# Kernel optimization log

Measured on AMD Instinct MI355X. Metric: run time of the kernel, lower is better.

The kernel has to match this reference:

```python
import jax, jax.numpy as jnp
import numpy as np

# Model constants (match init_kwargs + mamba_ssm defaults)
CIN, COUT, K, STRIDE = 64, 128, 4, 4
D = 128            # d_model = features_out
DI = 256           # d_inner = 2*D (expand=2)
NSTATE = 16        # d_state
DCONV = 4          # depthwise conv width
DT_RANK = 8        # ceil(D/16)
NB = 3             # blocks per direction
NTOT = 2 * NB      # forward + backward stacks


def setup_inputs() -> dict:
    key = jax.random.key(0)
    ks = jax.random.split(key, 10)
    s = 0.02
    x = jax.random.normal(ks[0], (2, CIN, 8192), jnp.float32)
    convd_w = jax.random.normal(ks[1], (COUT, CIN, K), jnp.float32) * s
    convd_b = jnp.zeros((COUT,), jnp.float32)
    ln_w = jnp.ones((NTOT, D), jnp.float32)
    ln_b = jnp.zeros((NTOT, D), jnp.float32)
    in_proj_w = jax.random.normal(ks[2], (NTOT, 2 * DI, D), jnp.float32) * s
    conv_w = jax.random.normal(ks[3], (NTOT, DI, DCONV), jnp.float32) * s
    conv_b = jnp.zeros((NTOT, DI), jnp.float32)
    xproj_w = jax.random.normal(ks[4], (NTOT, DT_RANK + 2 * NSTATE, DI), jnp.float32) * s
    dtproj_w = jax.random.normal(ks[5], (NTOT, DI, DT_RANK), jnp.float32) * s
    dtproj_b = jax.random.normal(ks[6], (NTOT, DI), jnp.float32) * s
    # S4D-real init: A = -[1..N]
    A_log = jnp.log(jnp.broadcast_to(jnp.arange(1, NSTATE + 1, dtype=jnp.float32), (NTOT, DI, NSTATE)))
    Dparam = jnp.ones((NTOT, DI), jnp.float32)
    outproj_w = jax.random.normal(ks[7], (NTOT, D, DI), jnp.float32) * s
    return dict(x=x, convd_w=convd_w, convd_b=convd_b, ln_w=ln_w, ln_b=ln_b,
                in_proj_w=in_proj_w, conv_w=conv_w, conv_b=conv_b, xproj_w=xproj_w,
                dtproj_w=dtproj_w, dtproj_b=dtproj_b, A_log=A_log, Dparam=Dparam,
                outproj_w=outproj_w)


def _silu(x):
    return x * jax.nn.sigmoid(x)


def _layernorm(x, w, b, eps=1e-5):
    m = x.mean(-1, keepdims=True)
    xc = x - m
    v = (xc * xc).mean(-1, keepdims=True)
    return xc * jax.lax.rsqrt(v + eps) * w + b


def _mamba_mixer(x, in_proj_w, conv_w, conv_b, xproj_w, dtproj_w, dtproj_b, A_log, Dp, outproj_w):
    # x: (B, L, D)
    B, L, _ = x.shape
    xz = jnp.einsum('bld,ed->ble', x, in_proj_w)          # (B, L, 2*DI)
    xm, z = jnp.split(xz, 2, axis=-1)
    # causal depthwise conv (pad left DCONV-1, truncate to L)
    xp = jnp.pad(xm, ((0, 0), (DCONV - 1, 0), (0, 0)))
    xc = conv_b
    acc = jnp.zeros_like(xm)
    for k in range(DCONV):
        acc = acc + xp[:, k:k + L, :] * conv_w[:, k]
    xc = _silu(acc + conv_b)                               # (B, L, DI)
    dbc = jnp.einsum('ble,ne->bln', xc, xproj_w)           # (B, L, DT_RANK + 2N)
    dt, Bc, Cc = jnp.split(dbc, [DT_RANK, DT_RANK + NSTATE], axis=-1)
    dt = jax.nn.softplus(jnp.einsum('blr,dr->bld', dt, dtproj_w) + dtproj_b)  # (B, L, DI)
    A = -jnp.exp(A_log)                                    # (DI, N)
    dA = jnp.exp(dt[..., None] * A)                        # (B, L, DI, N)
    dBx = dt[..., None] * Bc[:, :, None, :] * xc[..., None]

    def step(h, inp):
        dA_t, dBx_t, C_t = inp
        h = dA_t * h + dBx_t                               # (B, DI, N)
        y = jnp.einsum('bdn,bn->bd', h, C_t)
        return h, y

    h0 = jnp.zeros((B, DI, NSTATE), x.dtype)
    _, ys = jax.lax.scan(step, h0, (jnp.swapaxes(dA, 0, 1), jnp.swapaxes(dBx, 0, 1), jnp.swapaxes(Cc, 0, 1)))
    y = jnp.swapaxes(ys, 0, 1)                             # (B, L, DI)
    y = (y + Dp * xc) * _silu(z)
    return jnp.einsum('ble,de->bld', y, outproj_w)         # (B, L, D)


def _mamba_stack(x, off, ln_w, ln_b, in_proj_w, conv_w, conv_b, xproj_w, dtproj_w, dtproj_b, A_log, Dparam, outproj_w):
    # mamba_ssm Block semantics: residual = x (+ prev residual); x = mixer(norm(residual))
    res = None
    cur = x
    for i in range(NB):
        j = off + i
        res = cur if res is None else cur + res
        hn = _layernorm(res, ln_w[j], ln_b[j])
        cur = _mamba_mixer(hn, in_proj_w[j], conv_w[j], conv_b[j], xproj_w[j],
                           dtproj_w[j], dtproj_b[j], A_log[j], Dparam[j], outproj_w[j])
    return cur, res


def reference(x, convd_w, convd_b, ln_w, ln_b, in_proj_w, conv_w, conv_b, xproj_w,
              dtproj_w, dtproj_b, A_log, Dparam, outproj_w):
    # downsampling conv + SiLU
    y = jax.lax.conv_general_dilated(x, convd_w, (STRIDE,), 'VALID',
                                     dimension_numbers=('NCH', 'OIH', 'NCH'))
    y = _silu(y + convd_b[None, :, None])                  # (B, COUT, L')
    h = jnp.swapaxes(y, 1, 2)                              # (B, L', D)
    xf, rf = _mamba_stack(h, 0, ln_w, ln_b, in_proj_w, conv_w, conv_b, xproj_w,
                          dtproj_w, dtproj_b, A_log, Dparam, outproj_w)
    xb, rb = _mamba_stack(h[:, ::-1, :], NB, ln_w, ln_b, in_proj_w, conv_w, conv_b, xproj_w,
                          dtproj_w, dtproj_b, A_log, Dparam, outproj_w)
    out = (xf + rf) + (xb + rb)[:, ::-1, :]
    return jnp.swapaxes(out, 1, 2), rf, rb
```

## Files before the change

kernel.cpp:

```cpp
#include <hip/hip_runtime.h>
#include <hip/hip_bf16.h>
#include <math.h>

#define B    2
#define CIN  64
#define LIN  8192
#define L    2048
#define D    128
#define DI   256
#define NS   16
#define RK   8
#define NSTREAM 4
#define CH   32
#define NCH  (L/CH)
#define TOK  (NSTREAM*L)
#define SZ_D ((size_t)TOK*D)
#define SZ_DI ((size_t)TOK*DI)
#define SXM 280
#define SHN 152

typedef short  bfrag __attribute__((ext_vector_type(8)));
typedef float  facc  __attribute__((ext_vector_type(4)));
#define MFMA __builtin_amdgcn_mfma_f32_16x16x32_bf16

__device__ __forceinline__ float sigmoidf_(float x){ return 1.f/(1.f+__expf(-x)); }
__device__ __forceinline__ float siluf_(float x){ return x*sigmoidf_(x); }
__device__ __forceinline__ ushort f2bf(float f){
    unsigned u = __float_as_uint(f);
    u += 0x7fffu + ((u>>16)&1u);
    return (ushort)(u>>16);
}
__device__ __forceinline__ float bf2f(ushort u){ return __uint_as_float(((unsigned)u)<<16); }
__device__ __forceinline__ float softplusf_(float t){
    return (t > 20.f) ? t : __logf(1.f + __expf(t));
}

__global__ void k_cvtall(const float* __restrict__ cw, const float* __restrict__ ipw,
                         const float* __restrict__ opw, const float* __restrict__ xpw,
                         ushort* __restrict__ dst){
    int i = blockIdx.x*256 + threadIdx.x;
    ushort v;
    if (i < 32768)       v = f2bf(cw[i]);
    else if (i < 425984) v = f2bf(ipw[i-32768]);
    else if (i < 622592) v = f2bf(opw[i-425984]);
    else {
        int t = i - 622592;
        int k = t & 255, nr = (t>>8) & 63, j = t>>14;
        v = (nr < 40) ? f2bf(xpw[((size_t)j*40 + nr)*256 + k]) : (ushort)0;
    }
    dst[i] = v;
}

__global__ void k_down(const float* __restrict__ x, const ushort* __restrict__ wd,
                       const float* __restrict__ bias, float* __restrict__ h){
    __shared__ ushort sxd[64*SXM];
    int tid = threadIdx.x;
    int m0 = blockIdx.x*64;
    int b = m0 >> 11;
    int l0 = m0 & 2047;
    for (int idx = tid; idx < 64*64; idx += 256){
        int t = idx & 63, cc = idx >> 6;
        float4 v = *(const float4*)(x + ((size_t)(b*CIN + cc))*LIN + 4*(l0+t));
        ushort4 o; o.x=f2bf(v.x); o.y=f2bf(v.y); o.z=f2bf(v.z); o.w=f2bf(v.w);
        *(ushort4*)&sxd[t*SXM + cc*4] = o;
    }
    __syncthreads();
    int w = tid>>6, lane = tid&63, rw = w>>1, cw = w&1;
    int q = lane>>4, r = lane&15;
    int n0 = blockIdx.y*64 + cw*32;
    const ushort* b0p = wd + (size_t)(n0 + r)*256 + q*8;
    const ushort* b1p = b0p + (size_t)16*256;
    facc acc[2][2] = {};
    #pragma unroll
    for (int kb=0; kb<8; ++kb){
        bfrag a0 = *(bfrag*)&sxd[(rw*32 + r)*SXM + kb*32 + q*8];
        bfrag a1 = *(bfrag*)&sxd[(rw*32 + 16 + r)*SXM + kb*32 + q*8];
        bfrag b0 = *(const bfrag*)(b0p + kb*32);
        bfrag b1 = *(const bfrag*)(b1p + kb*32);
        acc[0][0] = MFMA(a0,b0,acc[0][0],0,0,0);
        acc[0][1] = MFMA(a0,b1,acc[0][1],0,0,0);
        acc[1][0] = MFMA(a1,b0,acc[1][0],0,0,0);
        acc[1][1] = MFMA(a1,b1,acc[1][1],0,0,0);
    }
    #pragma unroll
    for (int im=0; im<2; ++im)
    #pragma unroll
    for (int in=0; in<2; ++in){
        int col = n0 + in*16 + r;
        float bv = bias[col];
        #pragma unroll
        for (int r2=0; r2<4; ++r2){
            int row = m0 + rw*32 + im*16 + q*4 + r2;
            int bb = row >> 11, l = row & 2047;
            float v = siluf_(acc[im][in][r2] + bv);
            h[((size_t)(bb*L + l))*D + col] = v;
            h[((size_t)((2+bb)*L + (L-1-l)))*D + col] = v;
        }
    }
}

__global__ void __launch_bounds__(256,1)
k_head(const float* __restrict__ curIn, const float* __restrict__ resIn,
       float* __restrict__ resOut,
       const float* __restrict__ lnw, const float* __restrict__ lnb,
       const ushort* __restrict__ wbi, const ushort* __restrict__ wbx,
       const float* __restrict__ cw, const float* __restrict__ cb,
       const float* __restrict__ Wdt, const float* __restrict__ bdt,
       const float* __restrict__ A_log,
       float* __restrict__ z, float* __restrict__ xc,
       float* __restrict__ dtr, float* __restrict__ Bc, float* __restrict__ Cc,
       float* __restrict__ Aprod, float* __restrict__ Bend, int blk, int first){
    __shared__ ushort smHn[35*SHN];
    __shared__ ushort smXm[35*SXM];
    __shared__ ushort smXc[32*SXM];
    __shared__ float  smDbc[32*68];
    const int tid = threadIdx.x;
    const int bi = blockIdx.x;
    const int s = bi >> 6, c = bi & 63;
    const int j = (s>>1)*3 + blk;
    const int base_tok = s*L + c*CH;

    {
        int t = tid >> 3, g8 = tid & 7;
        size_t off = (size_t)(base_tok + t)*D + g8*16;
        float4 v[4];
        const float4* cp = (const float4*)(curIn + off);
        #pragma unroll
        for (int i=0;i<4;++i) v[i] = cp[i];
        if (!first){
            const float4* rp = (const float4*)(resIn + off);
            #pragma unroll
            for (int i=0;i<4;++i){ float4 rv=rp[i]; v[i].x+=rv.x; v[i].y+=rv.y; v[i].z+=rv.z; v[i].w+=rv.w; }
        }
        {
            float4* ro = (float4*)(resOut + off);
            #pragma unroll
            for (int i=0;i<4;++i) ro[i] = v[i];
        }
        float s1=0.f, s2=0.f;
        #pragma unroll
        for (int i=0;i<4;++i){
            s1 += v[i].x+v[i].y+v[i].z+v[i].w;
            s2 += v[i].x*v[i].x+v[i].y*v[i].y+v[i].z*v[i].z+v[i].w*v[i].w;
        }
        s1 += __shfl_xor(s1,1); s2 += __shfl_xor(s2,1);
        s1 += __shfl_xor(s1,2); s2 += __shfl_xor(s2,2);
        s1 += __shfl_xor(s1,4); s2 += __shfl_xor(s2,4);
        float mean = s1*(1.f/128.f);
        float var  = s2*(1.f/128.f) - mean*mean;
        float rstd = rsqrtf(var + 1e-5f);
        const float4* lwp = (const float4*)(lnw + j*D + g8*16);
        const float4* lbp = (const float4*)(lnb + j*D + g8*16);
        #pragma unroll
        for (int i=0;i<4;++i){
            float4 lw = lwp[i], lb = lbp[i];
            ushort4 o;
            o.x = f2bf((v[i].x-mean)*rstd*lw.x + lb.x);
            o.y = f2bf((v[i].y-mean)*rstd*lw.y + lb.y);
            o.z = f2bf((v[i].z-mean)*rstd*lw.z + lb.z);
            o.w = f2bf((v[i].w-mean)*rstd*lw.w + lb.w);
            *(ushort4*)&smHn[t*SHN + g8*16 + i*4] = o;
        }
    }
    if (c > 0 && tid < 24){
        int t = tid >> 3, g8 = tid & 7;
        size_t off = (size_t)(base_tok - 3 + t)*D + g8*16;
        float4 v[4];
        const float4* cp = (const float4*)(curIn + off);
        #pragma unroll
        for (int i=0;i<4;++i) v[i] = cp[i];
        if (!first){
            const float4* rp = (const float4*)(resIn + off);
            #pragma unroll
            for (int i=0;i<4;++i){ float4 rv=rp[i]; v[i].x+=rv.x; v[i].y+=rv.y; v[i].z+=rv.z; v[i].w+=rv.w; }
        }
        float s1=0.f, s2=0.f;
        #pragma unroll
        for (int i=0;i<4;++i){
            s1 += v[i].x+v[i].y+v[i].z+v[i].w;
            s2 += v[i].x*v[i].x+v[i].y*v[i].y+v[i].z*v[i].z+v[i].w*v[i].w;
        }
        s1 += __shfl_xor(s1,1); s2 += __shfl_xor(s2,1);
        s1 += __shfl_xor(s1,2); s2 += __shfl_xor(s2,2);
        s1 += __shfl_xor(s1,4); s2 += __shfl_xor(s2,4);
        float mean = s1*(1.f/128.f);
        float var  = s2*(1.f/128.f) - mean*mean;
        float rstd = rsqrtf(var + 1e-5f);
        const float4* lwp = (const float4*)(lnw + j*D + g8*16);
        const float4* lbp = (const float4*)(lnb + j*D + g8*16);
        #pragma unroll
        for (int i=0;i<4;++i){
            float4 lw = lwp[i], lb = lbp[i];
            ushort4 o;
            o.x = f2bf((v[i].x-mean)*rstd*lw.x + lb.x);
            o.y = f2bf((v[i].y-mean)*rstd*lw.y + lb.y);
            o.z = f2bf((v[i].z-mean)*rstd*lw.z + lb.z);
            o.w = f2bf((v[i].w-mean)*rstd*lw.w + lb.w);
            *(ushort4*)&smHn[(32+t)*SHN + g8*16 + i*4] = o;
        }
    }
    __syncthreads();

    {
        int w = tid>>6, lane = tid&63, q = lane>>4, r = lane&15;
        bfrag a[3][4];
        #pragma unroll
        for (int rt=0; rt<3; ++rt)
        #pragma unroll
        for (int kb=0; kb<4; ++kb)
            a[rt][kb] = *(bfrag*)&smHn[(rt*16 + r)*SHN + kb*32 + q*8];
        #pragma unroll
        for (int ct=0; ct<8; ++ct){
            int n0 = w*128 + ct*16;
            const ushort* bp = wbi + ((size_t)j*512 + n0 + r)*128 + q*8;
            facc a0 = {}, a1 = {}, a2 = {};
            #pragma unroll
            for (int kb=0; kb<4; ++kb){
                bfrag bv = *(const bfrag*)(bp + kb*32);
                a0 = MFMA(a[0][kb], bv, a0, 0,0,0);
                a1 = MFMA(a[1][kb], bv, a1, 0,0,0);
                a2 = MFMA(a[2][kb], bv, a2, 0,0,0);
            }
            int colL = n0 + r;
            if (colL < DI){
                #pragma unroll
                for (int r2=0;r2<4;++r2){
                    int rr = q*4 + r2;
                    smXm[rr*SXM + colL]      = f2bf(a0[r2]);
                    smXm[(16+rr)*SXM + colL] = f2bf(a1[r2]);
                    if (rr < 3) smXm[(32+rr)*SXM + colL] = f2bf(a2[r2]);
                }
            } else {
                int cz = colL - DI;
                #pragma unroll
                for (int r2=0;r2<4;++r2){
                    int rr = q*4 + r2;
                    z[(size_t)(base_tok + rr)*DI + cz]      = a0[r2];
                    z[(size_t)(base_tok + 16 + rr)*DI + cz] = a1[r2];
                }
            }
        }
    }
    __syncthreads();

    {
        const float* w4 = cw + ((size_t)j*DI + tid)*4;
        float cw0=w4[0], cw1=w4[1], cw2=w4[2], cw3=w4[3];
        float cbb = cb[j*DI + tid];
        float xm1=0.f, xm2=0.f, xm3=0.f;
        if (c > 0){
            xm3 = bf2f(smXm[32*SXM + tid]);
            xm2 = bf2f(smXm[33*SXM + tid]);
            xm1 = bf2f(smXm[34*SXM + tid]);
        }
        #pragma unroll 4
        for (int i=0;i<CH;++i){
            float x0 = bf2f(smXm[i*SXM + tid]);
            float v = siluf_(cbb + cw3*x0 + cw2*xm1 + cw1*xm2 + cw0*xm3);
            smXc[i*SXM + tid] = f2bf(v);
            xc[(size_t)(base_tok+i)*DI + tid] = v;
            xm3 = xm2; xm2 = xm1; xm1 = x0;
        }
    }
    __syncthreads();

    {
        int w = tid>>6, lane = tid&63, q = lane>>4, r = lane&15;
        facc a0 = {}, a1 = {};
        const ushort* bp = wbx + ((size_t)j*64 + w*16 + r)*256 + q*8;
        #pragma unroll
        for (int kb=0; kb<8; ++kb){
            bfrag av0 = *(bfrag*)&smXc[r*SXM + kb*32 + q*8];
            bfrag av1 = *(bfrag*)&smXc[(16+r)*SXM + kb*32 + q*8];
            bfrag bv  = *(const bfrag*)(bp + kb*32);
            a0 = MFMA(av0, bv, a0, 0,0,0);
            a1 = MFMA(av1, bv, a1, 0,0,0);
        }
        int col = w*16 + r;
        #pragma unroll
        for (int r2=0;r2<4;++r2){
            int rr = q*4 + r2;
            smDbc[rr*68 + col]      = a0[r2];
            smDbc[(16+rr)*68 + col] = a1[r2];
            int row0 = base_tok + rr, row1 = base_tok + 16 + rr;
            if      (col < 8){  dtr[(size_t)row0*RK + col] = a0[r2];      dtr[(size_t)row1*RK + col] = a1[r2]; }
            else if (col < 24){ Bc [(size_t)row0*NS + (col-8)] = a0[r2];  Bc [(size_t)row1*NS + (col-8)] = a1[r2]; }
            else if (col < 40){ Cc [(size_t)row0*NS + (col-24)] = a0[r2]; Cc [(size_t)row1*NS + (col-24)] = a1[r2]; }
        }
    }
    __syncthreads();

    {
        float A[NS], wv[RK];
        const float* ar = A_log + ((size_t)j*DI + tid)*NS;
        #pragma unroll
        for (int n=0;n<NS;++n) A[n] = -__expf(ar[n]);
        const float* wr = Wdt + ((size_t)j*DI + tid)*RK;
        #pragma unroll
        for (int r=0;r<RK;++r) wv[r] = wr[r];
        float bb2 = bdt[j*DI + tid];
        float ap[NS], hs[NS];
        #pragma unroll
        for (int n=0;n<NS;++n){ ap[n]=1.f; hs[n]=0.f; }
        #pragma unroll 4
        for (int l=0;l<CH;++l){
            float t = bb2;
            #pragma unroll
            for (int r=0;r<RK;++r) t += smDbc[l*68+r]*wv[r];
            float dtv = softplusf_(t);
            float xv  = bf2f(smXc[l*SXM + tid]);
            float dbx = dtv*xv;
            #pragma unroll
            for (int n=0;n<NS;++n){
                float dA = __expf(dtv*A[n]);
                ap[n] *= dA;
                hs[n] = dA*hs[n] + dbx*smDbc[l*68+8+n];
            }
        }
        size_t pb = (size_t)bi*4096 + tid;
        #pragma unroll
        for (int n=0;n<NS;++n){
            Aprod[pb + (size_t)n*256] = ap[n];
            Bend [pb + (size_t)n*256] = hs[n];
        }
    }
}

__global__ void k_scanmid(const float* __restrict__ Aprod, float* __restrict__ Bend){
    int tid = blockIdx.x*128 + threadIdx.x;
    int s = tid >> 12;
    int nd = tid & 4095;
    size_t base = (size_t)s*NCH*4096 + nd;
    float h = 0.f;
    for (int c0=0; c0<NCH; c0+=16){
        float a[16], b[16];
        #pragma unroll
        for (int i=0;i<16;++i){
            a[i] = Aprod[base + (size_t)(c0+i)*4096];
            b[i] = Bend [base + (size_t)(c0+i)*4096];
        }
        #pragma unroll
        for (int i=0;i<16;++i){
            Bend[base + (size_t)(c0+i)*4096] = h;
            h = a[i]*h + b[i];
        }
    }
}

__global__ void k_tail(const float* __restrict__ dtr, const float* __restrict__ xcv,
                       const float* __restrict__ Bc, const float* __restrict__ Cc,
                       const float* __restrict__ A_log,
                       const float* __restrict__ Wdt, const float* __restrict__ bdt,
                       const float* __restrict__ h0, const float* __restrict__ z,
                       const float* __restrict__ Dp, const ushort* __restrict__ wbo,
                       float* __restrict__ cur, int blk){
    int c = blockIdx.x, s = blockIdx.y; int j = (s>>1)*3 + blk;
    int d = threadIdx.x;
    __shared__ float sB[CH*NS], sC[CH*NS], sdtr[CH*RK];
    __shared__ ushort sg[CH*SXM];
    int base_tok = s*L + c*CH;
    sB[d] = Bc[(size_t)base_tok*NS + d];
    sB[256+d] = Bc[(size_t)base_tok*NS + 256 + d];
    sC[d] = Cc[(size_t)base_tok*NS + d];
    sC[256+d] = Cc[(size_t)base_tok*NS + 256 + d];
    sdtr[d] = dtr[(size_t)base_tok*RK + d];
    float A[NS], wv[RK];
    const float* ar = A_log + ((size_t)j*DI + d)*NS;
    #pragma unroll
    for (int n=0;n<NS;++n) A[n] = -__expf(ar[n]);
    const float* wr = Wdt + ((size_t)j*DI + d)*RK;
    #pragma unroll
    for (int r=0;r<RK;++r) wv[r] = wr[r];
    float bb = bdt[j*DI + d];
    float Dpd = Dp[j*DI + d];
    float hs[NS];
    size_t pb = (size_t)(s*NCH + c)*4096 + d;
    #pragma unroll
    for (int n=0;n<NS;++n) hs[n] = h0[pb + (size_t)n*256];
    __syncthreads();
    #pragma unroll 4
    for (int l=0;l<CH;++l){
        float t = bb;
        #pragma unroll
        for (int r=0;r<RK;++r) t += sdtr[l*RK+r]*wv[r];
        float dtv = softplusf_(t);
        float xv  = xcv[(size_t)(base_tok+l)*DI + d];
        float dbx = dtv*xv;
        float p = 0.f;
        #pragma unroll
        for (int n=0;n<NS;++n){
            float dA = __expf(dtv*A[n]);
            hs[n] = dA*hs[n] + dbx*sB[l*NS+n];
            p += hs[n]*sC[l*NS+n];
        }
        float zv = z[(size_t)(base_tok+l)*DI + d];
        sg[l*SXM + d] = f2bf((p + Dpd*xv)*siluf_(zv));
    }
    __syncthreads();
    int w = d>>6, lane = d&63, q = lane>>4, r = lane&15;
    facc acc[2][2] = {};
    const ushort* b0p = wbo + ((size_t)j*128 + w*32 + r)*256 + q*8;
    const ushort* b1p = b0p + 16*256;
    #pragma unroll
    for (int kb=0; kb<8; ++kb){
        bfrag av0 = *(bfrag*)&sg[r*SXM + kb*32 + q*8];
        bfrag av1 = *(bfrag*)&sg[(16+r)*SXM + kb*32 + q*8];
        bfrag bv0 = *(const bfrag*)(b0p + kb*32);
        bfrag bv1 = *(const bfrag*)(b1p + kb*32);
        acc[0][0] = MFMA(av0,bv0,acc[0][0],0,0,0);
        acc[0][1] = MFMA(av0,bv1,acc[0][1],0,0,0);
        acc[1][0] = MFMA(av1,bv0,acc[1][0],0,0,0);
        acc[1][1] = MFMA(av1,bv1,acc[1][1],0,0,0);
    }
    #pragma unroll
    for (int rt=0; rt<2; ++rt)
    #pragma unroll
    for (int ct=0; ct<2; ++ct){
        int col = w*32 + ct*16 + r;
        #pragma unroll
        for (int r2=0;r2<4;++r2){
            int row = base_tok + rt*16 + q*4 + r2;
            cur[(size_t)row*D + col] = acc[rt][ct][r2];
        }
    }
}

__global__ void k_final(const float* __restrict__ cur, const float* __restrict__ res,
                        float* __restrict__ out){
    int l = blockIdx.x, b = blockIdx.y, d = threadIdx.x;
    int tf = (b*L + l)*D + d;
    int tbk = ((2+b)*L + (L-1-l))*D + d;
    float f  = cur[tf] + res[tf];
    float bw = cur[tbk] + res[tbk];
    out[((size_t)(b*D + d))*L + l] = f + bw;
    out[(size_t)2*D*L + (size_t)(b*L + l)*D + d] = res[tf];
    out[(size_t)2*D*L + (size_t)((2+b)*L + l)*D + d] = res[((2+b)*L + l)*D + d];
}

extern "C" void kernel_launch(void* const* d_in, const int* in_sizes, int n_in,
                              void* d_out, int out_size, void* d_ws, size_t ws_size,
                              hipStream_t stream){
    const float* x         = (const float*)d_in[0];
    const float* convd_w   = (const float*)d_in[1];
    const float* convd_b   = (const float*)d_in[2];
    const float* ln_w      = (const float*)d_in[3];
    const float* ln_b      = (const float*)d_in[4];
    const float* in_proj_w = (const float*)d_in[5];
    const float* conv_w    = (const float*)d_in[6];
    const float* conv_b    = (const float*)d_in[7];
    const float* xproj_w   = (const float*)d_in[8];
    const float* dtproj_w  = (const float*)d_in[9];
    const float* dtproj_b  = (const float*)d_in[10];
    const float* A_log     = (const float*)d_in[11];
    const float* Dparam    = (const float*)d_in[12];
    const float* outproj_w = (const float*)d_in[13];

    float* ws = (float*)d_ws;
    float* h     = ws; ws += SZ_D;
    float* res0  = ws; ws += SZ_D;
    float* res1  = ws; ws += SZ_D;
    float* cur   = ws; ws += SZ_D;
    float* z     = ws; ws += SZ_DI;
    float* xc    = ws; ws += SZ_DI;
    float* Aprod = ws; ws += SZ_D;
    float* Bend  = ws; ws += SZ_D;
    float* dtr   = ws; ws += (size_t)TOK*RK;
    float* Bc    = ws; ws += (size_t)TOK*NS;
    float* Cc    = ws; ws += (size_t)TOK*NS;
    ushort* wall = (ushort*)ws;
    ushort* wbd  = wall;
    ushort* wbi  = wall + 32768;
    ushort* wbo  = wall + 425984;
    ushort* wbx  = wall + 622592;

    k_cvtall<<<2816, 256, 0, stream>>>(convd_w, in_proj_w, outproj_w, xproj_w, wall);
    k_down<<<dim3(64, 2), 256, 0, stream>>>(x, wbd, convd_b, h);

    float* resin[3]  = { nullptr, res0, res1 };
    float* resout[3] = { res0,    res1, res0 };
    for (int blk = 0; blk < 3; ++blk){
        const float* ci = (blk==0) ? h : cur;
        const float* ri = (blk==0) ? h : resin[blk];
        k_head<<<NSTREAM*NCH, 256, 0, stream>>>(ci, ri, resout[blk], ln_w, ln_b, wbi, wbx,
                                                conv_w, conv_b, dtproj_w, dtproj_b, A_log,
                                                z, xc, dtr, Bc, Cc, Aprod, Bend, blk, blk==0);
        k_scanmid<<<128, 128, 0, stream>>>(Aprod, Bend);
        k_tail<<<dim3(NCH, NSTREAM), 256, 0, stream>>>(dtr, xc, Bc, Cc, A_log,
                                                       dtproj_w, dtproj_b, Bend, z,
                                                       Dparam, wbo, cur, blk);
    }

    k_final<<<dim3(L, B), 128, 0, stream>>>(cur, res0, (float*)d_out);
}
```

Before: 254.4 us.

## Fuse downsample conv into first head, store z/xc as bf16, tile final transpose

Removes the separate k_down kernel and instead computes the strided downsampling conv plus SiLU inside k_head on the first block. Each chunk recomputes its own tokens plus a 3-token halo in shared memory, for both directions, so the h buffer is never written or read. The z and conv-output intermediates are stored as bf16 rather than fp32, halving their traffic, and k_tail preloads them into registers. k_final is rewritten with a shared-memory transpose for coalesced output writes and a vectorized residual copy. The trade-offs are redundant halo computation, bf16 rounding of z/xc that could shift accuracy, and higher register pressure in k_tail.

```diff
diff --git a/kernel.cpp b/kernel.cpp
--- a/kernel.cpp
+++ b/kernel.cpp
@@ -51,86 +51,90 @@
     dst[i] = v;
 }
 
-__global__ void k_down(const float* __restrict__ x, const ushort* __restrict__ wd,
-                       const float* __restrict__ bias, float* __restrict__ h){
-    __shared__ ushort sxd[64*SXM];
-    int tid = threadIdx.x;
-    int m0 = blockIdx.x*64;
-    int b = m0 >> 11;
-    int l0 = m0 & 2047;
-    for (int idx = tid; idx < 64*64; idx += 256){
-        int t = idx & 63, cc = idx >> 6;
-        float4 v = *(const float4*)(x + ((size_t)(b*CIN + cc))*LIN + 4*(l0+t));
-        ushort4 o; o.x=f2bf(v.x); o.y=f2bf(v.y); o.z=f2bf(v.z); o.w=f2bf(v.w);
-        *(ushort4*)&sxd[t*SXM + cc*4] = o;
-    }
-    __syncthreads();
-    int w = tid>>6, lane = tid&63, rw = w>>1, cw = w&1;
-    int q = lane>>4, r = lane&15;
-    int n0 = blockIdx.y*64 + cw*32;
-    const ushort* b0p = wd + (size_t)(n0 + r)*256 + q*8;
-    const ushort* b1p = b0p + (size_t)16*256;
-    facc acc[2][2] = {};
-    #pragma unroll
-    for (int kb=0; kb<8; ++kb){
-        bfrag a0 = *(bfrag*)&sxd[(rw*32 + r)*SXM + kb*32 + q*8];
-        bfrag a1 = *(bfrag*)&sxd[(rw*32 + 16 + r)*SXM + kb*32 + q*8];
-        bfrag b0 = *(const bfrag*)(b0p + kb*32);
-        bfrag b1 = *(const bfrag*)(b1p + kb*32);
-        acc[0][0] = MFMA(a0,b0,acc[0][0],0,0,0);
-        acc[0][1] = MFMA(a0,b1,acc[0][1],0,0,0);
-        acc[1][0] = MFMA(a1,b0,acc[1][0],0,0,0);
-        acc[1][1] = MFMA(a1,b1,acc[1][1],0,0,0);
-    }
-    #pragma unroll
-    for (int im=0; im<2; ++im)
-    #pragma unroll
-    for (int in=0; in<2; ++in){
-        int col = n0 + in*16 + r;
-        float bv = bias[col];
-        #pragma unroll
-        for (int r2=0; r2<4; ++r2){
-            int row = m0 + rw*32 + im*16 + q*4 + r2;
-            int bb = row >> 11, l = row & 2047;
-            float v = siluf_(acc[im][in][r2] + bv);
-            h[((size_t)(bb*L + l))*D + col] = v;
-            h[((size_t)((2+bb)*L + (L-1-l)))*D + col] = v;
-        }
-    }
-}
-
 __global__ void __launch_bounds__(256,1)
-k_head(const float* __restrict__ curIn, const float* __restrict__ resIn,
+k_head(const float* __restrict__ x,
+       const float* __restrict__ curIn, const float* __restrict__ resIn,
        float* __restrict__ resOut,
        const float* __restrict__ lnw, const float* __restrict__ lnb,
-       const ushort* __restrict__ wbi, const ushort* __restrict__ wbx,
+       const ushort* __restrict__ wbd, const ushort* __restrict__ wbi,
+       const ushort* __restrict__ wbx,
+       const float* __restrict__ dbias,
        const float* __restrict__ cw, const float* __restrict__ cb,
        const float* __restrict__ Wdt, const float* __restrict__ bdt,
        const float* __restrict__ A_log,
-       float* __restrict__ z, float* __restrict__ xc,
+       ushort* __restrict__ zb, ushort* __restrict__ xcb,
        float* __restrict__ dtr, float* __restrict__ Bc, float* __restrict__ Cc,
        float* __restrict__ Aprod, float* __restrict__ Bend, int blk, int first){
     __shared__ ushort smHn[35*SHN];
     __shared__ ushort smXm[35*SXM];
     __shared__ ushort smXc[32*SXM];
     __shared__ float  smDbc[32*68];
+    __shared__ float  smF[35*132];
     const int tid = threadIdx.x;
     const int bi = blockIdx.x;
     const int s = bi >> 6, c = bi & 63;
     const int j = (s>>1)*3 + blk;
     const int base_tok = s*L + c*CH;
 
+    if (first){
+        int bB = s & 1, dir = s >> 1;
+        for (int idx = tid; idx < 2240; idx += 256){
+            int rr = idx >> 6, cc = idx & 63;
+            int tl; bool valid = true;
+            if (rr < 32) tl = c*CH + rr;
+            else { tl = c*CH - 3 + (rr - 32); valid = (c > 0); }
+            if (valid){
+                int lo = dir ? (L-1-tl) : tl;
+                float4 v = *(const float4*)(x + ((size_t)(bB*CIN + cc))*LIN + 4*lo);
+                ushort4 o; o.x=f2bf(v.x); o.y=f2bf(v.y); o.z=f2bf(v.z); o.w=f2bf(v.w);
+                *(ushort4*)&smXm[rr*SXM + cc*4] = o;
+            }
+        }
+        __syncthreads();
+        int w = tid>>6, lane = tid&63, q = lane>>4, r = lane&15;
+        #pragma unroll
+        for (int ct=0; ct<2; ++ct){
+            int n0 = w*32 + ct*16;
+            const ushort* bp = wbd + (size_t)(n0 + r)*256 + q*8;
+            facc A0 = {}, A1 = {}, A2 = {};
+            #pragma unroll
+            for (int kb=0; kb<8; ++kb){
+                bfrag bv = *(const bfrag*)(bp + kb*32);
+                bfrag a0 = *(bfrag*)&smXm[r*SXM + kb*32 + q*8];
+                bfrag a1 = *(bfrag*)&smXm[(16+r)*SXM + kb*32 + q*8];
+                bfrag a2 = *(bfrag*)&smXm[(32+r)*SXM + kb*32 + q*8];
+                A0 = MFMA(a0,bv,A0,0,0,0);
+                A1 = MFMA(a1,bv,A1,0,0,0);
+                A2 = MFMA(a2,bv,A2,0,0,0);
+            }
+            float bvv = dbias[n0 + r];
+            #pragma unroll
+            for (int r2=0; r2<4; ++r2){
+                int rr2 = q*4 + r2;
+                smF[rr2*132 + n0 + r]      = siluf_(A0[r2] + bvv);
+                smF[(16+rr2)*132 + n0 + r] = siluf_(A1[r2] + bvv);
+                if (rr2 < 3) smF[(32+rr2)*132 + n0 + r] = siluf_(A2[r2] + bvv);
+            }
+        }
+        __syncthreads();
+    }
+
     {
         int t = tid >> 3, g8 = tid & 7;
         size_t off = (size_t)(base_tok + t)*D + g8*16;
         float4 v[4];
-        const float4* cp = (const float4*)(curIn + off);
-        #pragma unroll
-        for (int i=0;i<4;++i) v[i] = cp[i];
-        if (!first){
+        if (first){
+            #pragma unroll
+            for (int i=0;i<4;++i) v[i] = *(float4*)&smF[t*132 + g8*16 + i*4];
+        } else {
+            const float4* cp = (const float4*)(curIn + off);
             const float4* rp = (const float4*)(resIn + off);
             #pragma unroll
-            for (int i=0;i<4;++i){ float4 rv=rp[i]; v[i].x+=rv.x; v[i].y+=rv.y; v[i].z+=rv.z; v[i].w+=rv.w; }
+            for (int i=0;i<4;++i){
+                v[i] = cp[i];
+                float4 rv = rp[i];
+                v[i].x+=rv.x; v[i].y+=rv.y; v[i].z+=rv.z; v[i].w+=rv.w;
+            }
         }
         {
             float4* ro = (float4*)(resOut + off);
@@ -166,13 +170,18 @@
         int t = tid >> 3, g8 = tid & 7;
         size_t off = (size_t)(base_tok - 3 + t)*D + g8*16;
         float4 v[4];
-        const float4* cp = (const float4*)(curIn + off);
-        #pragma unroll
-        for (int i=0;i<4;++i) v[i] = cp[i];
-        if (!first){
+        if (first){
+            #pragma unroll
+            for (int i=0;i<4;++i) v[i] = *(float4*)&smF[(32+t)*132 + g8*16 + i*4];
+        } else {
+            const float4* cp = (const float4*)(curIn + off);
             const float4* rp = (const float4*)(resIn + off);
             #pragma unroll
-            for (int i=0;i<4;++i){ float4 rv=rp[i]; v[i].x+=rv.x; v[i].y+=rv.y; v[i].z+=rv.z; v[i].w+=rv.w; }
+            for (int i=0;i<4;++i){
+                v[i] = cp[i];
+                float4 rv = rp[i];
+                v[i].x+=rv.x; v[i].y+=rv.y; v[i].z+=rv.z; v[i].w+=rv.w;
+            }
         }
         float s1=0.f, s2=0.f;
         #pragma unroll
@@ -235,8 +244,8 @@
                 #pragma unroll
                 for (int r2=0;r2<4;++r2){
                     int rr = q*4 + r2;
-                    z[(size_t)(base_tok + rr)*DI + cz]      = a0[r2];
-                    z[(size_t)(base_tok + 16 + rr)*DI + cz] = a1[r2];
+                    zb[(size_t)(base_tok + rr)*DI + cz]      = f2bf(a0[r2]);
+                    zb[(size_t)(base_tok + 16 + rr)*DI + cz] = f2bf(a1[r2]);
                 }
             }
         }
@@ -257,8 +266,9 @@
         for (int i=0;i<CH;++i){
             float x0 = bf2f(smXm[i*SXM + tid]);
             float v = siluf_(cbb + cw3*x0 + cw2*xm1 + cw1*xm2 + cw0*xm3);
-            smXc[i*SXM + tid] = f2bf(v);
-            xc[(size_t)(base_tok+i)*DI + tid] = v;
+            ushort us = f2bf(v);
+            smXc[i*SXM + tid] = us;
+            xcb[(size_t)(base_tok+i)*DI + tid] = us;
             xm3 = xm2; xm2 = xm1; xm1 = x0;
         }
     }
@@ -347,11 +357,11 @@
     }
 }
 
-__global__ void k_tail(const float* __restrict__ dtr, const float* __restrict__ xcv,
+__global__ void k_tail(const float* __restrict__ dtr, const ushort* __restrict__ xcb,
                        const float* __restrict__ Bc, const float* __restrict__ Cc,
                        const float* __restrict__ A_log,
                        const float* __restrict__ Wdt, const float* __restrict__ bdt,
-                       const float* __restrict__ h0, const float* __restrict__ z,
+                       const float* __restrict__ h0, const ushort* __restrict__ zb,
                        const float* __restrict__ Dp, const ushort* __restrict__ wbo,
                        float* __restrict__ cur, int blk){
     int c = blockIdx.x, s = blockIdx.y; int j = (s>>1)*3 + blk;
@@ -359,11 +369,17 @@
     __shared__ float sB[CH*NS], sC[CH*NS], sdtr[CH*RK];
     __shared__ ushort sg[CH*SXM];
     int base_tok = s*L + c*CH;
-    sB[d] = Bc[(size_t)base_tok*NS + d];
+    ushort xvv[CH], zvv[CH];
+    #pragma unroll
+    for (int l=0;l<CH;++l){
+        xvv[l] = xcb[(size_t)(base_tok+l)*DI + d];
+        zvv[l] = zb [(size_t)(base_tok+l)*DI + d];
+    }
+    sB[d]     = Bc[(size_t)base_tok*NS + d];
     sB[256+d] = Bc[(size_t)base_tok*NS + 256 + d];
-    sC[d] = Cc[(size_t)base_tok*NS + d];
+    sC[d]     = Cc[(size_t)base_tok*NS + d];
     sC[256+d] = Cc[(size_t)base_tok*NS + 256 + d];
-    sdtr[d] = dtr[(size_t)base_tok*RK + d];
+    sdtr[d]   = dtr[(size_t)base_tok*RK + d];
     float A[NS], wv[RK];
     const float* ar = A_log + ((size_t)j*DI + d)*NS;
     #pragma unroll
@@ -384,7 +400,7 @@
         #pragma unroll
         for (int r=0;r<RK;++r) t += sdtr[l*RK+r]*wv[r];
         float dtv = softplusf_(t);
-        float xv  = xcv[(size_t)(base_tok+l)*DI + d];
+        float xv  = bf2f(xvv[l]);
         float dbx = dtv*xv;
         float p = 0.f;
         #pragma unroll
@@ -393,7 +409,7 @@
             hs[n] = dA*hs[n] + dbx*sB[l*NS+n];
             p += hs[n]*sC[l*NS+n];
         }
-        float zv = z[(size_t)(base_tok+l)*DI + d];
+        float zv = bf2f(zvv[l]);
         sg[l*SXM + d] = f2bf((p + Dpd*xv)*siluf_(zv));
     }
     __syncthreads();
@@ -427,14 +443,41 @@
 
 __global__ void k_final(const float* __restrict__ cur, const float* __restrict__ res,
                         float* __restrict__ out){
-    int l = blockIdx.x, b = blockIdx.y, d = threadIdx.x;
-    int tf = (b*L + l)*D + d;
-    int tbk = ((2+b)*L + (L-1-l))*D + d;
-    float f  = cur[tf] + res[tf];
-    float bw = cur[tbk] + res[tbk];
-    out[((size_t)(b*D + d))*L + l] = f + bw;
-    out[(size_t)2*D*L + (size_t)(b*L + l)*D + d] = res[tf];
-    out[(size_t)2*D*L + (size_t)((2+b)*L + l)*D + d] = res[((2+b)*L + l)*D + d];
+    __shared__ float tile[128*33];
+    int tid = threadIdx.x;
+    int c = blockIdx.x, b = blockIdx.y;
+    int t = tid>>3, g8 = tid&7;
+    int lf = c*32 + t, lb = L-1-lf;
+    size_t fo = ((size_t)(b*L + lf))*D + g8*16;
+    size_t bo = ((size_t)((2+b)*L + lb))*D + g8*16;
+    #pragma unroll
+    for (int i=0;i<4;++i){
+        float4 cf  = *(const float4*)(cur + fo + i*4);
+        float4 rf  = *(const float4*)(res + fo + i*4);
+        float4 cb2 = *(const float4*)(cur + bo + i*4);
+        float4 rb2 = *(const float4*)(res + bo + i*4);
+        int db = g8*16 + i*4;
+        tile[(db+0)*33 + t] = cf.x+rf.x+cb2.x+rb2.x;
+        tile[(db+1)*33 + t] = cf.y+rf.y+cb2.y+rb2.y;
+        tile[(db+2)*33 + t] = cf.z+rf.z+cb2.z+rb2.z;
+        tile[(db+3)*33 + t] = cf.w+rf.w+cb2.w+rb2.w;
+    }
+    __syncthreads();
+    int d = tid>>1, hf = tid&1;
+    size_t obase = ((size_t)(b*D + d))*L + c*32 + hf*16;
+    #pragma unroll
+    for (int i=0;i<4;++i){
+        float4 o4;
+        o4.x = tile[d*33 + hf*16 + i*4 + 0];
+        o4.y = tile[d*33 + hf*16 + i*4 + 1];
+        o4.z = tile[d*33 + hf*16 + i*4 + 2];
+        o4.w = tile[d*33 + hf*16 + i*4 + 3];
+        *(float4*)(out + obase + i*4) = o4;
+    }
+    const float4* src = (const float4*)res;
+    float4* dst = (float4*)(out + (size_t)2*D*L);
+    for (int idx = (blockIdx.y*NCH + blockIdx.x)*256 + tid; idx < 262144; idx += 2*NCH*256)
+        dst[idx] = src[idx];
 }
 
 extern "C" void kernel_launch(void* const* d_in, const int* in_sizes, int n_in,
@@ -456,17 +499,16 @@
     const float* outproj_w = (const float*)d_in[13];
 
     float* ws = (float*)d_ws;
-    float* h     = ws; ws += SZ_D;
     float* res0  = ws; ws += SZ_D;
     float* res1  = ws; ws += SZ_D;
     float* cur   = ws; ws += SZ_D;
-    float* z     = ws; ws += SZ_DI;
-    float* xc    = ws; ws += SZ_DI;
     float* Aprod = ws; ws += SZ_D;
     float* Bend  = ws; ws += SZ_D;
     float* dtr   = ws; ws += (size_t)TOK*RK;
     float* Bc    = ws; ws += (size_t)TOK*NS;
     float* Cc    = ws; ws += (size_t)TOK*NS;
+    ushort* zb   = (ushort*)ws; ws += SZ_DI/2;
+    ushort* xcb  = (ushort*)ws; ws += SZ_DI/2;
     ushort* wall = (ushort*)ws;
     ushort* wbd  = wall;
     ushort* wbi  = wall + 32768;
@@ -474,21 +516,21 @@
     ushort* wbx  = wall + 622592;
 
     k_cvtall<<<2816, 256, 0, stream>>>(convd_w, in_proj_w, outproj_w, xproj_w, wall);
-    k_down<<<dim3(64, 2), 256, 0, stream>>>(x, wbd, convd_b, h);
 
     float* resin[3]  = { nullptr, res0, res1 };
     float* resout[3] = { res0,    res1, res0 };
     for (int blk = 0; blk < 3; ++blk){
-        const float* ci = (blk==0) ? h : cur;
-        const float* ri = (blk==0) ? h : resin[blk];
-        k_head<<<NSTREAM*NCH, 256, 0, stream>>>(ci, ri, resout[blk], ln_w, ln_b, wbi, wbx,
+        const float* ci = (blk==0) ? nullptr : cur;
+        const float* ri = (blk==0) ? nullptr : resin[blk];
+        k_head<<<NSTREAM*NCH, 256, 0, stream>>>(x, ci, ri, resout[blk], ln_w, ln_b,
+                                                wbd, wbi, wbx, convd_b,
                                                 conv_w, conv_b, dtproj_w, dtproj_b, A_log,
-                                                z, xc, dtr, Bc, Cc, Aprod, Bend, blk, blk==0);
+                                                zb, xcb, dtr, Bc, Cc, Aprod, Bend, blk, blk==0);
         k_scanmid<<<128, 128, 0, stream>>>(Aprod, Bend);
-        k_tail<<<dim3(NCH, NSTREAM), 256, 0, stream>>>(dtr, xc, Bc, Cc, A_log,
-                                                       dtproj_w, dtproj_b, Bend, z,
+        k_tail<<<dim3(NCH, NSTREAM), 256, 0, stream>>>(dtr, xcb, Bc, Cc, A_log,
+                                                       dtproj_w, dtproj_b, Bend, zb,
                                                        Dparam, wbo, cur, blk);
     }
 
-    k_final<<<dim3(L, B), 128, 0, stream>>>(cur, res0, (float*)d_out);
-}
+    k_final<<<dim3(NCH, B), 256, 0, stream>>>(cur, res0, (float*)d_out);
+}
```

Measured after the change: 296.7 us. 16.6% more time.
